# Kernel tuning notes

Hardware: AMD Instinct MI355X
Metric: run time of the kernel (lower is better)

The kernel has to match this reference:

```python
import jax, jax.numpy as jnp
import numpy as np
import math

B, T, D = 2, 2048, 1024
N_EXP, TOP_K = 8, 2
CAP_FACTOR = 1.25  # train_capacity (module in training mode)
MIN_CAP = 4


def _capacity(num_tokens):
    cap = math.floor(TOP_K * CAP_FACTOR * num_tokens / N_EXP)
    cap += cap % 2
    return max(cap, MIN_CAP)


def setup_inputs() -> dict:
    key = jax.random.key(0)
    k1, k2 = jax.random.split(key)
    x = jax.random.normal(k1, (B, T, D), dtype=jnp.float32)
    w_g = jax.random.normal(k2, (N_EXP, D), dtype=jnp.float32) * 0.02
    return {"x": x, "w_g": w_g}


def reference(x, w_g):
    Bx, Tx, Dx = x.shape
    n_tok = Bx * Tx
    cap = _capacity(n_tok)  # static: depends only on shapes

    # router runs in full precision (router_use_full_prec=True)
    logits = jnp.einsum('btd,ed->bte', x.astype(jnp.float32), w_g.astype(jnp.float32))
    logits = logits.reshape(n_tok, N_EXP)

    top_v, top_i = jax.lax.top_k(logits, TOP_K)          # [n_tok, k]
    # softmax over (-inf)-masked logits == softmax over the k selected logits
    probs_k = jax.nn.softmax(top_v, axis=-1)             # [n_tok, k]

    # expert one-hot mask, ordered [k, tokens, n_exp] (matches torch permute)
    exp_mask = jax.nn.one_hot(top_i, N_EXP, dtype=jnp.int32)   # [n_tok, k, n_exp]
    exp_mask = jnp.transpose(exp_mask, (1, 0, 2))              # [k, n_tok, n_exp]

    # position-in-expert-queue rank via cumsum over flattened (k*tokens)
    rank = jnp.cumsum(exp_mask.reshape(TOP_K * n_tok, N_EXP), axis=0) - 1
    rank = rank.reshape(TOP_K, n_tok, N_EXP)

    exp_mask = exp_mask * (rank < cap).astype(jnp.int32)       # drop overflow tokens
    used_capacity = jnp.sum(exp_mask, axis=(0, 1))             # [n_exp]

    rank_sel = jnp.sum(exp_mask * rank, axis=-1)               # [k, n_tok] int
    keep = jnp.sum(exp_mask, axis=-1).astype(jnp.float32)      # [k, n_tok] 0/1
    w_sel = probs_k.T * keep                                   # [k, n_tok]

    # combine weights: scatter instead of the O(k*tok*n_exp*cap) outer product
    cb_weight = jnp.zeros((n_tok, N_EXP, cap), dtype=jnp.float32)
    tok_ids = jnp.arange(n_tok)
    for k in range(TOP_K):  # tiny static loop over top_k
        cb_weight = cb_weight.at[tok_ids, top_i[:, k], rank_sel[k]].add(w_sel[k])

    sec_mask = cb_weight != 0
    return used_capacity, cb_weight, sec_mask
```

## Files before the change

### kernel.cpp

```cpp
#include <hip/hip_runtime.h>

#define N_TOK   4096
#define DDIM    1024
#define N_EXP   8
#define CAP     1280
#define ROW     (N_EXP * CAP)
#define CB_ELEMS (N_TOK * ROW)

typedef __attribute__((ext_vector_type(4))) float f32x4;


__global__ __launch_bounds__(256) void router_kernel(
    const float* __restrict__ x, const float* __restrict__ wg,
    int* __restrict__ e0, int* __restrict__ e1,
    float* __restrict__ p0, float* __restrict__ p1)
{
    const int wave = threadIdx.x >> 6;
    const int lane = threadIdx.x & 63;
    const int t = blockIdx.x * 4 + wave;

    const float4* xt  = (const float4*)(x + (size_t)t * DDIM);
    const float4* wg4 = (const float4*)wg;

    float acc[N_EXP];
#pragma unroll
    for (int e = 0; e < N_EXP; ++e) acc[e] = 0.f;

#pragma unroll
    for (int it = 0; it < 4; ++it) {
        const int d4 = lane + it * 64;
        const float4 xv = xt[d4];
#pragma unroll
        for (int e = 0; e < N_EXP; ++e) {
            const float4 wv = wg4[e * 256 + d4];
            acc[e] = fmaf(xv.x, wv.x,
                     fmaf(xv.y, wv.y,
                     fmaf(xv.z, wv.z,
                     fmaf(xv.w, wv.w, acc[e]))));
        }
    }

#pragma unroll
    for (int e = 0; e < N_EXP; ++e) {
#pragma unroll
        for (int off = 32; off >= 1; off >>= 1)
            acc[e] += __shfl_xor(acc[e], off, 64);
    }

    if (lane == 0) {
        float v0 = -3.402823466e38f, v1 = -3.402823466e38f;
        int   i0 = 0, i1 = 0;
#pragma unroll
        for (int e = 0; e < N_EXP; ++e) {
            const float v = acc[e];
            if (v > v0)      { v1 = v0; i1 = i0; v0 = v; i0 = e; }
            else if (v > v1) { v1 = v;  i1 = e; }
        }
        const float ex  = expf(v1 - v0);
        const float inv = 1.f / (1.f + ex);
        e0[t] = i0;
        e1[t] = i1;
        p0[t] = inv;
        p1[t] = ex * inv;
    }
}

__global__ __launch_bounds__(1024) void scan_kernel(
    const int* __restrict__ e0, const int* __restrict__ e1,
    int2* __restrict__ r01, float* __restrict__ out)
{
    __shared__ int lds_e[2 * N_TOK];
    __shared__ int seg_cnt[16][N_EXP];
    __shared__ int seg_base[16][N_EXP];

    for (int i = threadIdx.x; i < N_TOK; i += 1024) {
        lds_e[i]         = e0[i];
        lds_e[N_TOK + i] = e1[i];
    }
    __syncthreads();

    const int s    = threadIdx.x >> 6;
    const int lane = threadIdx.x & 63;
    const unsigned long long lt = (1ull << lane) - 1ull;

    int cnt[N_EXP];
#pragma unroll
    for (int ex = 0; ex < N_EXP; ++ex) cnt[ex] = 0;
#pragma unroll
    for (int c = 0; c < 8; ++c) {
        const int e = lds_e[s * 512 + c * 64 + lane];
#pragma unroll
        for (int ex = 0; ex < N_EXP; ++ex)
            cnt[ex] += __popcll(__ballot(e == ex));
    }
    if (lane == 0) {
#pragma unroll
        for (int ex = 0; ex < N_EXP; ++ex) seg_cnt[s][ex] = cnt[ex];
    }
    __syncthreads();

    if (threadIdx.x < N_EXP) {
        int run = 0;
#pragma unroll
        for (int s2 = 0; s2 < 16; ++s2) {
            seg_base[s2][threadIdx.x] = run;
            run += seg_cnt[s2][threadIdx.x];
        }
        out[threadIdx.x] = (float)min(run, CAP);
    }
    __syncthreads();

    int run[N_EXP];
#pragma unroll
    for (int ex = 0; ex < N_EXP; ++ex) run[ex] = seg_base[s][ex];

#pragma unroll
    for (int c = 0; c < 8; ++c) {
        const int i = s * 512 + c * 64 + lane;
        const int e = lds_e[i];
        int myrank = 0;
#pragma unroll
        for (int ex = 0; ex < N_EXP; ++ex) {
            const unsigned long long bal = __ballot(e == ex);
            if (e == ex) myrank = run[ex] + __popcll(bal & lt);
            run[ex] += __popcll(bal);
        }
        const int er = (e << 16) | myrank;
        if (i < N_TOK) r01[i].x = er;
        else           r01[i - N_TOK].y = er;
    }
}

__global__ __launch_bounds__(256) void fill_kernel(
    const int2* __restrict__ r01, const float* __restrict__ p0,
    const float* __restrict__ p1, float* __restrict__ out)
{
    const int  b     = blockIdx.x;
    const bool is_cb = (b < 2048);
    const int  t0    = is_cb ? (b * 2) : ((b - 2048) * 2);

    float* base = out + 8 + (is_cb ? 0 : (size_t)CB_ELEMS) + (size_t)t0 * ROW;
    f32x4* b4   = (f32x4*)base;
    const f32x4 z = {0.f, 0.f, 0.f, 0.f};

#pragma unroll
    for (int it = 0; it < 20; ++it)
        b4[threadIdx.x + it * 256] = z;

    __syncthreads();

    if (threadIdx.x < 4) {
        const int  tt = t0 + (threadIdx.x >> 1);
        const int2 rr = r01[tt];
        const int  er = (threadIdx.x & 1) ? rr.y : rr.x;
        const int  r  = er & 0xFFFF;
        const int  e  = er >> 16;
        if (r < CAP) {
            const float w = (threadIdx.x & 1) ? p1[tt] : p0[tt];
            const float v = is_cb ? w : ((w != 0.f) ? 1.f : 0.f);
            base[(size_t)(tt - t0) * ROW + e * CAP + r] = v;
        }
    }
}

extern "C" void kernel_launch(void* const* d_in, const int* in_sizes, int n_in,
                              void* d_out, int out_size, void* d_ws, size_t ws_size,
                              hipStream_t stream)
{
    const float* x  = (const float*)d_in[0];
    const float* wg = (const float*)d_in[1];
    float* out = (float*)d_out;

    char*  ws  = (char*)d_ws;
    int*   e0  = (int*)(ws);
    int*   e1  = (int*)(ws + 16384);
    float* p0  = (float*)(ws + 32768);
    float* p1  = (float*)(ws + 49152);
    int2*  r01 = (int2*)(ws + 65536);

    router_kernel<<<N_TOK / 4, 256, 0, stream>>>(x, wg, e0, e1, p0, p1);
    scan_kernel<<<1, 1024, 0, stream>>>(e0, e1, r01, out);
    fill_kernel<<<4096, 256, 0, stream>>>(r01, p0, p1, out);
}
```

Measured before the change: 82.44 us.

## Remove scan kernel; pack expert ids as nibbles and compute ranks in fill

Drops the single-block scan kernel. The router now packs each token's top-2 expert indices into 4-bit fields. Each fill block loads the whole 4 KB packed array into LDS and counts earlier matching entries to get its own queue rank, and block 0 also computes the used-capacity counts. This removes a serialized single-workgroup launch and its dependency gap. In exchange, every fill block does redundant O(tokens) counting work.

```diff
diff --git a/kernel.cpp b/kernel.cpp
--- a/kernel.cpp
+++ b/kernel.cpp
@@ -12,9 +12,10 @@
 
 __global__ __launch_bounds__(256) void router_kernel(
     const float* __restrict__ x, const float* __restrict__ wg,
-    int* __restrict__ e0, int* __restrict__ e1,
+    unsigned int* __restrict__ pk,
     float* __restrict__ p0, float* __restrict__ p1)
 {
+    __shared__ int se0[4], se1[4];
     const int wave = threadIdx.x >> 6;
     const int lane = threadIdx.x & 63;
     const int t = blockIdx.x * 4 + wave;
@@ -58,86 +59,35 @@
         }
         const float ex  = expf(v1 - v0);
         const float inv = 1.f / (1.f + ex);
-        e0[t] = i0;
-        e1[t] = i1;
         p0[t] = inv;
         p1[t] = ex * inv;
-    }
-}
-
-__global__ __launch_bounds__(1024) void scan_kernel(
-    const int* __restrict__ e0, const int* __restrict__ e1,
-    int2* __restrict__ r01, float* __restrict__ out)
-{
-    __shared__ int lds_e[2 * N_TOK];
-    __shared__ int seg_cnt[16][N_EXP];
-    __shared__ int seg_base[16][N_EXP];
-
-    for (int i = threadIdx.x; i < N_TOK; i += 1024) {
-        lds_e[i]         = e0[i];
-        lds_e[N_TOK + i] = e1[i];
+        se0[wave] = i0;
+        se1[wave] = i1;
     }
     __syncthreads();
 
-    const int s    = threadIdx.x >> 6;
-    const int lane = threadIdx.x & 63;
-    const unsigned long long lt = (1ull << lane) - 1ull;
-
-    int cnt[N_EXP];
-#pragma unroll
-    for (int ex = 0; ex < N_EXP; ++ex) cnt[ex] = 0;
-#pragma unroll
-    for (int c = 0; c < 8; ++c) {
-        const int e = lds_e[s * 512 + c * 64 + lane];
-#pragma unroll
-        for (int ex = 0; ex < N_EXP; ++ex)
-            cnt[ex] += __popcll(__ballot(e == ex));
-    }
-    if (lane == 0) {
-#pragma unroll
-        for (int ex = 0; ex < N_EXP; ++ex) seg_cnt[s][ex] = cnt[ex];
-    }
-    __syncthreads();
-
-    if (threadIdx.x < N_EXP) {
-        int run = 0;
-#pragma unroll
-        for (int s2 = 0; s2 < 16; ++s2) {
-            seg_base[s2][threadIdx.x] = run;
-            run += seg_cnt[s2][threadIdx.x];
-        }
-        out[threadIdx.x] = (float)min(run, CAP);
-    }
-    __syncthreads();
-
-    int run[N_EXP];
-#pragma unroll
-    for (int ex = 0; ex < N_EXP; ++ex) run[ex] = seg_base[s][ex];
-
-#pragma unroll
-    for (int c = 0; c < 8; ++c) {
-        const int i = s * 512 + c * 64 + lane;
-        const int e = lds_e[i];
-        int myrank = 0;
-#pragma unroll
-        for (int ex = 0; ex < N_EXP; ++ex) {
-            const unsigned long long bal = __ballot(e == ex);
-            if (e == ex) myrank = run[ex] + __popcll(bal & lt);
-            run[ex] += __popcll(bal);
-        }
-        const int er = (e << 16) | myrank;
-        if (i < N_TOK) r01[i].x = er;
-        else           r01[i - N_TOK].y = er;
+    if (threadIdx.x == 0) {
+        const int b = blockIdx.x;
+        unsigned short* pks = (unsigned short*)pk;
+        const unsigned short h0 = (unsigned short)(se0[0] | (se0[1] << 4) |
+                                                   (se0[2] << 8) | (se0[3] << 12));
+        const unsigned short h1 = (unsigned short)(se1[0] | (se1[1] << 4) |
+                                                   (se1[2] << 8) | (se1[3] << 12));
+        pks[b]        = h0;
+        pks[1024 + b] = h1;
     }
 }
 
 __global__ __launch_bounds__(256) void fill_kernel(
-    const int2* __restrict__ r01, const float* __restrict__ p0,
+    const unsigned int* __restrict__ pk, const float* __restrict__ p0,
     const float* __restrict__ p1, float* __restrict__ out)
 {
+    __shared__ unsigned int spk[1024];
+    __shared__ int s_e[4], s_r[4];
+
     const int  b     = blockIdx.x;
     const bool is_cb = (b < 2048);
-    const int  t0    = is_cb ? (b * 2) : ((b - 2048) * 2);
+    const int  t0    = (is_cb ? b : (b - 2048)) * 2;
 
     float* base = out + 8 + (is_cb ? 0 : (size_t)CB_ELEMS) + (size_t)t0 * ROW;
     f32x4* b4   = (f32x4*)base;
@@ -147,18 +97,56 @@
     for (int it = 0; it < 20; ++it)
         b4[threadIdx.x + it * 256] = z;
 
+#pragma unroll
+    for (int j = 0; j < 4; ++j)
+        spk[threadIdx.x + j * 256] = pk[threadIdx.x + j * 256];
+    __syncthreads();
+
+    const int wave = threadIdx.x >> 6;
+    const int lane = threadIdx.x & 63;
+
+    const int tt = t0 + (wave >> 1);
+    const int i  = (wave & 1) * N_TOK + tt;
+    const int e  = (spk[i >> 3] >> ((i & 7) * 4)) & 0xF;
+
+    int cnt = 0;
+    for (int j = 0; j < 16; ++j) {
+        const unsigned int w  = spk[lane + j * 64];
+        const int          bi = (lane + j * 64) * 8;
+#pragma unroll
+        for (int s = 0; s < 8; ++s)
+            cnt += (bi + s < i && (int)((w >> (4 * s)) & 0xF) == e) ? 1 : 0;
+    }
+#pragma unroll
+    for (int off = 32; off >= 1; off >>= 1)
+        cnt += __shfl_xor(cnt, off, 64);
+
+    if (lane == 0) { s_e[wave] = e; s_r[wave] = cnt; }
     __syncthreads();
 
     if (threadIdx.x < 4) {
-        const int  tt = t0 + (threadIdx.x >> 1);
-        const int2 rr = r01[tt];
-        const int  er = (threadIdx.x & 1) ? rr.y : rr.x;
-        const int  r  = er & 0xFFFF;
-        const int  e  = er >> 16;
+        const int r = s_r[threadIdx.x];
         if (r < CAP) {
-            const float w = (threadIdx.x & 1) ? p1[tt] : p0[tt];
-            const float v = is_cb ? w : ((w != 0.f) ? 1.f : 0.f);
-            base[(size_t)(tt - t0) * ROW + e * CAP + r] = v;
+            const int   tt2 = t0 + (threadIdx.x >> 1);
+            const float w   = (threadIdx.x & 1) ? p1[tt2] : p0[tt2];
+            const float v   = is_cb ? w : ((w != 0.f) ? 1.f : 0.f);
+            base[(size_t)(tt2 - t0) * ROW + s_e[threadIdx.x] * CAP + r] = v;
+        }
+    }
+
+    if (b == 0) {
+        for (int ee = wave * 2; ee < wave * 2 + 2; ++ee) {
+            int c = 0;
+            for (int j = 0; j < 16; ++j) {
+                const unsigned int w = spk[lane + j * 64];
+#pragma unroll
+                for (int s = 0; s < 8; ++s)
+                    c += ((int)((w >> (4 * s)) & 0xF) == ee) ? 1 : 0;
+            }
+#pragma unroll
+            for (int off = 32; off >= 1; off >>= 1)
+                c += __shfl_xor(c, off, 64);
+            if (lane == 0) out[ee] = (float)min(c, CAP);
         }
     }
 }
@@ -171,14 +159,11 @@
     const float* wg = (const float*)d_in[1];
     float* out = (float*)d_out;
 
-    char*  ws  = (char*)d_ws;
-    int*   e0  = (int*)(ws);
-    int*   e1  = (int*)(ws + 16384);
-    float* p0  = (float*)(ws + 32768);
-    float* p1  = (float*)(ws + 49152);
-    int2*  r01 = (int2*)(ws + 65536);
+    char*         ws = (char*)d_ws;
+    unsigned int* pk = (unsigned int*)(ws);
+    float*        p0 = (float*)(ws + 4096);
+    float*        p1 = (float*)(ws + 20480);
 
-    router_kernel<<<N_TOK / 4, 256, 0, stream>>>(x, wg, e0, e1, p0, p1);
-    scan_kernel<<<1, 1024, 0, stream>>>(e0, e1, r01, out);
-    fill_kernel<<<4096, 256, 0, stream>>>(r01, p0, p1, out);
+    router_kernel<<<N_TOK / 4, 256, 0, stream>>>(x, wg, pk, p0, p1);
+    fill_kernel<<<4096, 256, 0, stream>>>(pk, p0, p1, out);
 }
```

After: 75.81 us, median of 2. 1.09x faster.
